# Optimization experiments

Measured on AMD Instinct MI355X. Metric: run time of the kernel, lower is better.

Reference implementation:

```python
import jax, jax.numpy as jnp
import numpy as np
import math

NUM_HEADS = 16
HEAD_DIM = 64
EMBED = 1024
NUM_BUCKETS = 32
MAX_DISTANCE = 128


def _relative_position_bucket(relative_position, num_buckets=NUM_BUCKETS, max_distance=MAX_DISTANCE):
    # bidirectional T5 bucketing
    nb = num_buckets // 2
    relative_buckets = (relative_position > 0).astype(jnp.int32) * nb
    rp = jnp.abs(relative_position)
    max_exact = nb // 2
    is_small = rp < max_exact
    rp_safe = jnp.maximum(rp, 1)  # avoid log(0); masked by is_small anyway
    rp_large = max_exact + (
        jnp.log(rp_safe.astype(jnp.float32) / max_exact)
        / math.log(max_distance / max_exact)
        * (nb - max_exact)
    ).astype(jnp.int32)
    rp_large = jnp.minimum(rp_large, nb - 1)
    return relative_buckets + jnp.where(is_small, rp, rp_large)


def compute_bias(rel_emb, q_len, k_len):
    ctx = jnp.arange(q_len)[:, None]
    mem = jnp.arange(k_len)[None, :]
    buckets = _relative_position_bucket(mem - ctx)  # [q,k]
    values = rel_emb[buckets]                       # [q,k,H]
    return jnp.transpose(values, (2, 0, 1))[None]   # [1,H,q,k]


def setup_inputs() -> dict:
    key = jax.random.key(0)
    ks = jax.random.split(key, 6)
    std = 0.02
    B, S = 2, 2048
    inner = NUM_HEADS * HEAD_DIM
    return {
        "input_ids": jax.random.normal(ks[0], (B, S, EMBED), dtype=jnp.float32),
        "Wq": jax.random.normal(ks[1], (EMBED, inner), dtype=jnp.float32) * std,
        "Wk": jax.random.normal(ks[2], (EMBED, inner), dtype=jnp.float32) * std,
        "Wv": jax.random.normal(ks[3], (EMBED, inner), dtype=jnp.float32) * std,
        "Wo": jax.random.normal(ks[4], (inner, EMBED), dtype=jnp.float32) * std,
        "rel_emb": jax.random.normal(ks[5], (NUM_BUCKETS, NUM_HEADS), dtype=jnp.float32) * std,
    }


def reference(input_ids, Wq, Wk, Wv, Wo, rel_emb):
    B, S, _ = input_ids.shape
    H, D = NUM_HEADS, HEAD_DIM
    q = (input_ids @ Wq).reshape(B, S, H, D).transpose(0, 2, 1, 3)  # [B,H,S,D]
    k = (input_ids @ Wk).reshape(B, S, H, D).transpose(0, 2, 1, 3)
    v = (input_ids @ Wv).reshape(B, S, H, D).transpose(0, 2, 1, 3)
    scores = jnp.einsum("bhqd,bhkd->bhqk", q, k)  # no 1/sqrt(d) scaling (T5 style)
    position_bias = compute_bias(rel_emb, S, S)   # [1,H,S,S]
    scores = scores + position_bias
    attn = jax.nn.softmax(scores, axis=-1)
    out = jnp.einsum("bhqk,bhkd->bhqd", attn, v)
    out = out.transpose(0, 2, 1, 3).reshape(B, S, H * D)
    out = out @ Wo
    return out, position_bias
```

## Files before the change

kernel.cpp:

```cpp
#include <hip/hip_runtime.h>
#include <stdint.h>

#define S_LEN 2048
#define NH 16
#define EMB 1024

typedef __attribute__((ext_vector_type(8))) short bf16x8;
typedef __attribute__((ext_vector_type(4))) float floatx4;
typedef const __attribute__((address_space(1))) unsigned int* gas_u32p;
typedef __attribute__((address_space(3))) unsigned int* las_u32p;

static __device__ __forceinline__ void gld_lds16(const void* g, void* l) {
  __builtin_amdgcn_global_load_lds((gas_u32p)g, (las_u32p)l, 16, 0, 0);
}

static __device__ __forceinline__ unsigned short f2bf(float f) {
  unsigned int u = __float_as_uint(f);
  unsigned int r = (u + 0x7FFFu + ((u >> 16) & 1u)) >> 16;
  return (unsigned short)r;
}

__global__ void cast_x_kernel(const float* __restrict__ x, unsigned short* __restrict__ out, int n4) {
  int i = blockIdx.x * blockDim.x + threadIdx.x;
  if (i >= n4) return;
  float4 v = ((const float4*)x)[i];
  ushort4 o;
  o.x = f2bf(v.x); o.y = f2bf(v.y); o.z = f2bf(v.z); o.w = f2bf(v.w);
  ((ushort4*)out)[i] = o;
}

__global__ void transpose_cast3(const float* __restrict__ W0, const float* __restrict__ W1,
                                const float* __restrict__ W2, unsigned short* __restrict__ out) {
  __shared__ float tile[32][33];
  const float* in = (blockIdx.z == 0) ? W0 : ((blockIdx.z == 1) ? W1 : W2);
  unsigned short* o = out + (size_t)blockIdx.z * 1048576;
  int x = blockIdx.x * 32 + threadIdx.x;
  int y0 = blockIdx.y * 32 + threadIdx.y;
#pragma unroll
  for (int j = 0; j < 4; j++)
    tile[threadIdx.y + 8 * j][threadIdx.x] = in[(y0 + 8 * j) * EMB + x];
  __syncthreads();
  int x2 = blockIdx.y * 32 + threadIdx.x;
  int y2 = blockIdx.x * 32 + threadIdx.y;
#pragma unroll
  for (int j = 0; j < 4; j++)
    o[(y2 + 8 * j) * EMB + x2] = f2bf(tile[threadIdx.x][threadIdx.y + 8 * j]);
}

__global__ void build_lut_kernel(const float* __restrict__ rel_emb, float* __restrict__ lut) {
  int idx = blockIdx.x * blockDim.x + threadIdx.x;
  if (idx >= 4096) return;
  int delta = idx - 2048;
  int bucket = (delta > 0) ? 16 : 0;
  int rp = (delta < 0) ? -delta : delta;
  int bl;
  if (rp < 8) bl = rp;
  else bl = 8 + (rp >= 12) + (rp >= 16) + (rp >= 23) + (rp >= 32) + (rp >= 46) + (rp >= 64) + (rp >= 91);
  bucket += bl;
#pragma unroll
  for (int h = 0; h < NH; h++)
    lut[h * 4096 + idx] = rel_emb[bucket * NH + h];
}

__global__ void bias_out_kernel(const float* __restrict__ lut, float* __restrict__ dst) {
  int i = blockIdx.x * blockDim.x + threadIdx.x;
  int h = i >> 20;
  int rem = i & 1048575;
  int q = rem >> 9;
  int k4 = (rem & 511) << 2;
  const float* lr = lut + h * 4096 + (k4 - q + 2048);
  float4 v = make_float4(__ldg(lr), __ldg(lr + 1), __ldg(lr + 2), __ldg(lr + 3));
  ((float4*)dst)[i] = v;
}

template <int MODE>
__global__ __launch_bounds__(256) void gemm2(const unsigned short* __restrict__ A,
                                             const unsigned short* __restrict__ BT,
                                             unsigned short* __restrict__ oQ,
                                             unsigned short* __restrict__ oK,
                                             unsigned short* __restrict__ oV,
                                             float* __restrict__ oF) {
  __shared__ __align__(16) unsigned short As[128 * 64];
  __shared__ __align__(16) unsigned short Bs[128 * 64];
  const int tid = threadIdx.x;
  const int wave = tid >> 6, lane = tid & 63;
  const int quad = lane >> 4, lm = lane & 15;
  const int wm = wave & 1, wn = wave >> 1;
  const int mBase = blockIdx.y * 128, nBase = blockIdx.x * 128;
  const int gg = (lane & 7) ^ (lane >> 3);
  const int srow = lane >> 3;
  floatx4 acc[4][4];
#pragma unroll
  for (int i = 0; i < 4; i++)
#pragma unroll
    for (int j = 0; j < 4; j++) acc[i][j] = (floatx4){0.f, 0.f, 0.f, 0.f};

  for (int kt = 0; kt < 16; kt++) {
    int k0 = kt * 64;
    __syncthreads();
#pragma unroll
    for (int c = 0; c < 4; c++) {
      int chunk = wave * 4 + c;
      int row = chunk * 8 + srow;
      gld_lds16(&A[(size_t)(mBase + row) * 1024 + k0 + gg * 8], &As[chunk * 512]);
      gld_lds16(&BT[(size_t)(nBase + row) * 1024 + k0 + gg * 8], &Bs[chunk * 512]);
    }
    __syncthreads();
#pragma unroll
    for (int hh = 0; hh < 2; hh++) {
      bf16x8 af[4], bfr[4];
#pragma unroll
      for (int i = 0; i < 4; i++)
        af[i] = *(const bf16x8*)&As[(wm * 64 + i * 16 + lm) * 64 + (((hh << 2) + quad) ^ (lm & 7)) * 8];
#pragma unroll
      for (int j = 0; j < 4; j++)
        bfr[j] = *(const bf16x8*)&Bs[(wn * 64 + j * 16 + lm) * 64 + (((hh << 2) + quad) ^ (lm & 7)) * 8];
#pragma unroll
      for (int i = 0; i < 4; i++)
#pragma unroll
        for (int j = 0; j < 4; j++)
          acc[i][j] = __builtin_amdgcn_mfma_f32_16x16x32_bf16(af[i], bfr[j], acc[i][j], 0, 0, 0);
    }
  }
  const int which = nBase >> 10;
#pragma unroll
  for (int i = 0; i < 4; i++) {
#pragma unroll
    for (int j = 0; j < 4; j++) {
#pragma unroll
      for (int r = 0; r < 4; r++) {
        int row = mBase + wm * 64 + i * 16 + quad * 4 + r;
        int col = nBase + wn * 64 + j * 16 + lm;
        float v = acc[i][j][r];
        if (MODE == 1) {
          oF[(size_t)row * 1024 + col] = v;
        } else {
          int b = row >> 11, s = row & 2047;
          int cw = col & 1023;
          int h = cw >> 6, d = cw & 63;
          if (which == 0)      oQ[(((size_t)(b * NH + h) * S_LEN + s) * 64) + d] = f2bf(v);
          else if (which == 1) oK[(((size_t)(b * NH + h) * S_LEN + s) * 64) + d] = f2bf(v);
          else                 oV[(((size_t)(b * NH + h) * 64 + d) * S_LEN) + s] = f2bf(v);
        }
      }
    }
  }
}

__global__ __launch_bounds__(256) void attn_kernel(const unsigned short* __restrict__ Qb,
                                                   const unsigned short* __restrict__ Kb,
                                                   const unsigned short* __restrict__ Vtb,
                                                   const float* __restrict__ lut,
                                                   unsigned short* __restrict__ Ob) {
  __shared__ __align__(16) unsigned short Kl[64 * 64];
  __shared__ __align__(16) unsigned short Vl[64 * 64];
  __shared__ __align__(16) unsigned short Pl[4 * 16 * 72];
  const int tid = threadIdx.x;
  const int wave = tid >> 6, lane = tid & 63;
  const int quad = lane >> 4, lm = lane & 15;
  const int h = blockIdx.y, b = blockIdx.z;
  const int bh = b * NH + h;
  const int qTile = blockIdx.x * 128;
  const unsigned short* Qp = Qb + (size_t)bh * S_LEN * 64;
  const unsigned short* Kp = Kb + (size_t)bh * S_LEN * 64;
  const unsigned short* Vp = Vtb + (size_t)bh * 64 * S_LEN;
  const float* lrow = lut + h * 4096;
  const float cneg = lrow[0], cpos = lrow[4095];
  const int gg = (lane & 7) ^ (lane >> 3);
  const int srow = lane >> 3;
  const int qw = qTile + wave * 32;

  bf16x8 aq[2][2];
#pragma unroll
  for (int g = 0; g < 2; g++)
#pragma unroll
    for (int hh = 0; hh < 2; hh++)
      aq[g][hh] = *(const bf16x8*)&Qp[(qw + g * 16 + lm) * 64 + hh * 32 + quad * 8];

  floatx4 accO[2][4];
#pragma unroll
  for (int g = 0; g < 2; g++)
#pragma unroll
    for (int d = 0; d < 4; d++) accO[g][d] = (floatx4){0.f, 0.f, 0.f, 0.f};
  float lp[2] = {0.f, 0.f};

  unsigned short* Pw = &Pl[wave * 16 * 72];

  for (int kt = 0; kt < 32; kt++) {
    int kBase = kt * 64;
    __syncthreads();
#pragma unroll
    for (int c = 0; c < 2; c++) {
      int chunk = wave * 2 + c;
      int row = chunk * 8 + srow;
      gld_lds16(&Kp[(size_t)(kBase + row) * 64 + gg * 8], &Kl[chunk * 512]);
      gld_lds16(&Vp[(size_t)row * S_LEN + kBase + gg * 8], &Vl[chunk * 512]);
    }
    __syncthreads();

    bf16x8 kf[4][2], vf[4][2];
#pragma unroll
    for (int nt = 0; nt < 4; nt++)
#pragma unroll
      for (int hh = 0; hh < 2; hh++) {
        int off = (nt * 16 + lm) * 64 + (((hh << 2) + quad) ^ (lm & 7)) * 8;
        kf[nt][hh] = *(const bf16x8*)&Kl[off];
        vf[nt][hh] = *(const bf16x8*)&Vl[off];
      }

    bool farTile = (kBase + 154 <= qTile) || (kBase >= qTile + 218);
    float cfar = (kBase < qTile) ? cneg : cpos;

#pragma unroll
    for (int g = 0; g < 2; g++) {
      int q = qw + g * 16 + lm;
      floatx4 s4[4];
#pragma unroll
      for (int nt = 0; nt < 4; nt++) {
        floatx4 z = (floatx4){0.f, 0.f, 0.f, 0.f};
        z = __builtin_amdgcn_mfma_f32_16x16x32_bf16(kf[nt][0], aq[g][0], z, 0, 0, 0);
        z = __builtin_amdgcn_mfma_f32_16x16x32_bf16(kf[nt][1], aq[g][1], z, 0, 0, 0);
        s4[nt] = z;
      }
      float psum = 0.f;
#pragma unroll
      for (int nt = 0; nt < 4; nt++) {
        union { unsigned short u[4]; uint2 v; } pk;
#pragma unroll
        for (int r = 0; r < 4; r++) {
          float sv;
          if (farTile) sv = s4[nt][r] + cfar;
          else {
            int kcol = kBase + nt * 16 + quad * 4 + r;
            sv = s4[nt][r] + __ldg(&lrow[kcol - q + 2048]);
          }
          float p = __expf(sv);
          psum += p;
          pk.u[r] = f2bf(p);
        }
        *(uint2*)&Pw[lm * 72 + nt * 16 + quad * 4] = pk.v;
      }
      lp[g] += psum;
      bf16x8 pa0 = *(const bf16x8*)&Pw[lm * 72 + quad * 8];
      bf16x8 pa1 = *(const bf16x8*)&Pw[lm * 72 + 32 + quad * 8];
#pragma unroll
      for (int d = 0; d < 4; d++) {
        accO[g][d] = __builtin_amdgcn_mfma_f32_16x16x32_bf16(pa0, vf[d][0], accO[g][d], 0, 0, 0);
        accO[g][d] = __builtin_amdgcn_mfma_f32_16x16x32_bf16(pa1, vf[d][1], accO[g][d], 0, 0, 0);
      }
    }
  }
#pragma unroll
  for (int g = 0; g < 2; g++) {
    lp[g] += __shfl_xor(lp[g], 16, 64);
    lp[g] += __shfl_xor(lp[g], 32, 64);
  }
#pragma unroll
  for (int g = 0; g < 2; g++) {
    float linv[4];
#pragma unroll
    for (int r = 0; r < 4; r++) linv[r] = 1.f / __shfl(lp[g], quad * 4 + r, 64);
#pragma unroll
    for (int d = 0; d < 4; d++)
#pragma unroll
      for (int r = 0; r < 4; r++) {
        int q = qw + g * 16 + quad * 4 + r;
        int col = h * 64 + d * 16 + lm;
        Ob[((size_t)(b * S_LEN + q)) * 1024 + col] = f2bf(accO[g][d][r] * linv[r]);
      }
  }
}

extern "C" void kernel_launch(void* const* d_in, const int* in_sizes, int n_in,
                              void* d_out, int out_size, void* d_ws, size_t ws_size,
                              hipStream_t stream) {
  const float* X   = (const float*)d_in[0];
  const float* Wq  = (const float*)d_in[1];
  const float* Wk  = (const float*)d_in[2];
  const float* Wv  = (const float*)d_in[3];
  const float* Wo  = (const float*)d_in[4];
  const float* rel = (const float*)d_in[5];
  float* out = (float*)d_out;
  float* bias_out = out + 4194304;

  char* ws = (char*)d_ws;
  unsigned short* Xb    = (unsigned short*)(ws);
  unsigned short* WqkvT = (unsigned short*)(ws + (size_t)(8u  << 20));
  unsigned short* WoT   = (unsigned short*)(ws + (size_t)(14u << 20));
  unsigned short* Qb    = (unsigned short*)(ws + (size_t)(16u << 20));
  unsigned short* Kb    = (unsigned short*)(ws + (size_t)(24u << 20));
  unsigned short* Vtb   = (unsigned short*)(ws + (size_t)(32u << 20));
  unsigned short* Ob    = (unsigned short*)(ws + (size_t)(40u << 20));
  float* lut            = (float*)(ws + (size_t)(48u << 20));

  cast_x_kernel<<<4096, 256, 0, stream>>>(X, Xb, 1048576);
  dim3 tb(32, 8);
  transpose_cast3<<<dim3(32, 32, 3), tb, 0, stream>>>(Wq, Wk, Wv, WqkvT);
  transpose_cast3<<<dim3(32, 32, 1), tb, 0, stream>>>(Wo, Wo, Wo, WoT);
  build_lut_kernel<<<16, 256, 0, stream>>>(rel, lut);
  bias_out_kernel<<<65536, 256, 0, stream>>>(lut, bias_out);

  gemm2<0><<<dim3(24, 32), 256, 0, stream>>>(Xb, WqkvT, Qb, Kb, Vtb, nullptr);
  attn_kernel<<<dim3(16, 16, 2), 256, 0, stream>>>(Qb, Kb, Vtb, lut, Ob);
  gemm2<1><<<dim3(8, 32), 256, 0, stream>>>(Ob, WoT, nullptr, nullptr, nullptr, out);
}
```

Measured before the change: 478.9 us.

## Fuse bias output into attention, split QKV GEMM, remap attention grid

Removes the standalone position-bias kernel. The batch-0 attention blocks now write the bias tile for each key block with nontemporal stores, using a constant fill for far tiles. The QKV GEMM is split into a Q/K kernel and a separate V kernel whose MFMA operands are swapped so the transposed V store is coalesced along s. Attention blocks are remapped to a 1D grid that interleaves batch and head, the P scratch pitch changes from 72 to 68, and a cheaper round-half-up bf16 conversion is used for P and O. Risks include extra store traffic inside attention for batch-0 blocks, load imbalance between the two batches, and slightly different rounding.

```diff
diff --git a/kernel.cpp b/kernel.cpp
--- a/kernel.cpp
+++ b/kernel.cpp
@@ -18,6 +18,9 @@
   unsigned int u = __float_as_uint(f);
   unsigned int r = (u + 0x7FFFu + ((u >> 16) & 1u)) >> 16;
   return (unsigned short)r;
+}
+static __device__ __forceinline__ unsigned short f2bf_fast(float f) {
+  return (unsigned short)((__float_as_uint(f) + 0x8000u) >> 16);
 }
 
 __global__ void cast_x_kernel(const float* __restrict__ x, unsigned short* __restrict__ out, int n4) {
@@ -62,24 +65,10 @@
     lut[h * 4096 + idx] = rel_emb[bucket * NH + h];
 }
 
-__global__ void bias_out_kernel(const float* __restrict__ lut, float* __restrict__ dst) {
-  int i = blockIdx.x * blockDim.x + threadIdx.x;
-  int h = i >> 20;
-  int rem = i & 1048575;
-  int q = rem >> 9;
-  int k4 = (rem & 511) << 2;
-  const float* lr = lut + h * 4096 + (k4 - q + 2048);
-  float4 v = make_float4(__ldg(lr), __ldg(lr + 1), __ldg(lr + 2), __ldg(lr + 3));
-  ((float4*)dst)[i] = v;
-}
-
-template <int MODE>
-__global__ __launch_bounds__(256) void gemm2(const unsigned short* __restrict__ A,
-                                             const unsigned short* __restrict__ BT,
-                                             unsigned short* __restrict__ oQ,
-                                             unsigned short* __restrict__ oK,
-                                             unsigned short* __restrict__ oV,
-                                             float* __restrict__ oF) {
+__global__ __launch_bounds__(256) void gemm_qk(const unsigned short* __restrict__ A,
+                                               const unsigned short* __restrict__ BT,
+                                               unsigned short* __restrict__ oQ,
+                                               unsigned short* __restrict__ oK) {
   __shared__ __align__(16) unsigned short As[128 * 64];
   __shared__ __align__(16) unsigned short Bs[128 * 64];
   const int tid = threadIdx.x;
@@ -124,43 +113,154 @@
   }
   const int which = nBase >> 10;
 #pragma unroll
-  for (int i = 0; i < 4; i++) {
-#pragma unroll
-    for (int j = 0; j < 4; j++) {
+  for (int i = 0; i < 4; i++)
+#pragma unroll
+    for (int j = 0; j < 4; j++)
 #pragma unroll
       for (int r = 0; r < 4; r++) {
         int row = mBase + wm * 64 + i * 16 + quad * 4 + r;
         int col = nBase + wn * 64 + j * 16 + lm;
-        float v = acc[i][j][r];
-        if (MODE == 1) {
-          oF[(size_t)row * 1024 + col] = v;
-        } else {
-          int b = row >> 11, s = row & 2047;
-          int cw = col & 1023;
-          int h = cw >> 6, d = cw & 63;
-          if (which == 0)      oQ[(((size_t)(b * NH + h) * S_LEN + s) * 64) + d] = f2bf(v);
-          else if (which == 1) oK[(((size_t)(b * NH + h) * S_LEN + s) * 64) + d] = f2bf(v);
-          else                 oV[(((size_t)(b * NH + h) * 64 + d) * S_LEN) + s] = f2bf(v);
-        }
-      }
-    }
-  }
+        int b = row >> 11, s = row & 2047;
+        int cw = col & 1023;
+        int h = cw >> 6, d = cw & 63;
+        unsigned short v = f2bf(acc[i][j][r]);
+        if (which == 0) oQ[(((size_t)(b * NH + h) * S_LEN + s) * 64) + d] = v;
+        else            oK[(((size_t)(b * NH + h) * S_LEN + s) * 64) + d] = v;
+      }
+}
+
+__global__ __launch_bounds__(256) void gemm_v(const unsigned short* __restrict__ A,
+                                              const unsigned short* __restrict__ BT,
+                                              unsigned short* __restrict__ oV) {
+  __shared__ __align__(16) unsigned short As[128 * 64];
+  __shared__ __align__(16) unsigned short Bs[128 * 64];
+  const int tid = threadIdx.x;
+  const int wave = tid >> 6, lane = tid & 63;
+  const int quad = lane >> 4, lm = lane & 15;
+  const int wm = wave & 1, wn = wave >> 1;
+  const int mBase = blockIdx.y * 128, nBase = blockIdx.x * 128;
+  const int gg = (lane & 7) ^ (lane >> 3);
+  const int srow = lane >> 3;
+  floatx4 acc[4][4];
+#pragma unroll
+  for (int i = 0; i < 4; i++)
+#pragma unroll
+    for (int j = 0; j < 4; j++) acc[i][j] = (floatx4){0.f, 0.f, 0.f, 0.f};
+
+  for (int kt = 0; kt < 16; kt++) {
+    int k0 = kt * 64;
+    __syncthreads();
+#pragma unroll
+    for (int c = 0; c < 4; c++) {
+      int chunk = wave * 4 + c;
+      int row = chunk * 8 + srow;
+      gld_lds16(&A[(size_t)(mBase + row) * 1024 + k0 + gg * 8], &As[chunk * 512]);
+      gld_lds16(&BT[(size_t)(nBase + row) * 1024 + k0 + gg * 8], &Bs[chunk * 512]);
+    }
+    __syncthreads();
+#pragma unroll
+    for (int hh = 0; hh < 2; hh++) {
+      bf16x8 af[4], bfr[4];
+#pragma unroll
+      for (int i = 0; i < 4; i++)
+        af[i] = *(const bf16x8*)&As[(wm * 64 + i * 16 + lm) * 64 + (((hh << 2) + quad) ^ (lm & 7)) * 8];
+#pragma unroll
+      for (int j = 0; j < 4; j++)
+        bfr[j] = *(const bf16x8*)&Bs[(wn * 64 + j * 16 + lm) * 64 + (((hh << 2) + quad) ^ (lm & 7)) * 8];
+#pragma unroll
+      for (int i = 0; i < 4; i++)
+#pragma unroll
+        for (int j = 0; j < 4; j++)
+          acc[i][j] = __builtin_amdgcn_mfma_f32_16x16x32_bf16(bfr[j], af[i], acc[i][j], 0, 0, 0);
+    }
+  }
+#pragma unroll
+  for (int i = 0; i < 4; i++)
+#pragma unroll
+    for (int j = 0; j < 4; j++)
+#pragma unroll
+      for (int r = 0; r < 4; r++) {
+        int n = nBase + wn * 64 + j * 16 + quad * 4 + r;
+        int m = mBase + wm * 64 + i * 16 + lm;
+        int h = n >> 6, d = n & 63;
+        int b = m >> 11, s = m & 2047;
+        oV[(((size_t)(b * NH + h) * 64 + d) * S_LEN) + s] = f2bf(acc[i][j][r]);
+      }
+}
+
+__global__ __launch_bounds__(256) void gemm_out(const unsigned short* __restrict__ A,
+                                                const unsigned short* __restrict__ BT,
+                                                float* __restrict__ oF) {
+  __shared__ __align__(16) unsigned short As[128 * 64];
+  __shared__ __align__(16) unsigned short Bs[128 * 64];
+  const int tid = threadIdx.x;
+  const int wave = tid >> 6, lane = tid & 63;
+  const int quad = lane >> 4, lm = lane & 15;
+  const int wm = wave & 1, wn = wave >> 1;
+  const int mBase = blockIdx.y * 128, nBase = blockIdx.x * 128;
+  const int gg = (lane & 7) ^ (lane >> 3);
+  const int srow = lane >> 3;
+  floatx4 acc[4][4];
+#pragma unroll
+  for (int i = 0; i < 4; i++)
+#pragma unroll
+    for (int j = 0; j < 4; j++) acc[i][j] = (floatx4){0.f, 0.f, 0.f, 0.f};
+
+  for (int kt = 0; kt < 16; kt++) {
+    int k0 = kt * 64;
+    __syncthreads();
+#pragma unroll
+    for (int c = 0; c < 4; c++) {
+      int chunk = wave * 4 + c;
+      int row = chunk * 8 + srow;
+      gld_lds16(&A[(size_t)(mBase + row) * 1024 + k0 + gg * 8], &As[chunk * 512]);
+      gld_lds16(&BT[(size_t)(nBase + row) * 1024 + k0 + gg * 8], &Bs[chunk * 512]);
+    }
+    __syncthreads();
+#pragma unroll
+    for (int hh = 0; hh < 2; hh++) {
+      bf16x8 af[4], bfr[4];
+#pragma unroll
+      for (int i = 0; i < 4; i++)
+        af[i] = *(const bf16x8*)&As[(wm * 64 + i * 16 + lm) * 64 + (((hh << 2) + quad) ^ (lm & 7)) * 8];
+#pragma unroll
+      for (int j = 0; j < 4; j++)
+        bfr[j] = *(const bf16x8*)&Bs[(wn * 64 + j * 16 + lm) * 64 + (((hh << 2) + quad) ^ (lm & 7)) * 8];
+#pragma unroll
+      for (int i = 0; i < 4; i++)
+#pragma unroll
+        for (int j = 0; j < 4; j++)
+          acc[i][j] = __builtin_amdgcn_mfma_f32_16x16x32_bf16(af[i], bfr[j], acc[i][j], 0, 0, 0);
+    }
+  }
+#pragma unroll
+  for (int i = 0; i < 4; i++)
+#pragma unroll
+    for (int j = 0; j < 4; j++)
+#pragma unroll
+      for (int r = 0; r < 4; r++) {
+        int row = mBase + wm * 64 + i * 16 + quad * 4 + r;
+        int col = nBase + wn * 64 + j * 16 + lm;
+        oF[(size_t)row * 1024 + col] = acc[i][j][r];
+      }
 }
 
 __global__ __launch_bounds__(256) void attn_kernel(const unsigned short* __restrict__ Qb,
                                                    const unsigned short* __restrict__ Kb,
                                                    const unsigned short* __restrict__ Vtb,
                                                    const float* __restrict__ lut,
-                                                   unsigned short* __restrict__ Ob) {
+                                                   unsigned short* __restrict__ Ob,
+                                                   float* __restrict__ bias_out) {
   __shared__ __align__(16) unsigned short Kl[64 * 64];
   __shared__ __align__(16) unsigned short Vl[64 * 64];
-  __shared__ __align__(16) unsigned short Pl[4 * 16 * 72];
+  __shared__ __align__(16) unsigned short Pl[4 * 16 * 68];
   const int tid = threadIdx.x;
   const int wave = tid >> 6, lane = tid & 63;
   const int quad = lane >> 4, lm = lane & 15;
-  const int h = blockIdx.y, b = blockIdx.z;
-  const int bh = b * NH + h;
-  const int qTile = blockIdx.x * 128;
+  const int ii = blockIdx.x;
+  const int bh = (ii & 7) * 4 + ((ii >> 3) & 3);
+  const int qTile = (ii >> 5) * 128;
+  const int b = bh >> 4, h = bh & 15;
   const unsigned short* Qp = Qb + (size_t)bh * S_LEN * 64;
   const unsigned short* Kp = Kb + (size_t)bh * S_LEN * 64;
   const unsigned short* Vp = Vtb + (size_t)bh * 64 * S_LEN;
@@ -169,6 +269,8 @@
   const int gg = (lane & 7) ^ (lane >> 3);
   const int srow = lane >> 3;
   const int qw = qTile + wave * 32;
+  const bool writeBias = (b == 0);
+  float* bdst = bias_out + ((size_t)(h * S_LEN + qTile)) * S_LEN;
 
   bf16x8 aq[2][2];
 #pragma unroll
@@ -184,7 +286,7 @@
     for (int d = 0; d < 4; d++) accO[g][d] = (floatx4){0.f, 0.f, 0.f, 0.f};
   float lp[2] = {0.f, 0.f};
 
-  unsigned short* Pw = &Pl[wave * 16 * 72];
+  unsigned short* Pw = &Pl[wave * 16 * 68];
 
   for (int kt = 0; kt < 32; kt++) {
     int kBase = kt * 64;
@@ -198,6 +300,31 @@
     }
     __syncthreads();
 
+    bool farTile = (kBase + 154 <= qTile) || (kBase >= qTile + 218);
+    float cfar = (kBase < qTile) ? cneg : cpos;
+
+    if (writeBias) {
+      float* bt = bdst + kBase;
+      if (farTile) {
+        floatx4 cf4 = (floatx4){cfar, cfar, cfar, cfar};
+#pragma unroll
+        for (int e = 0; e < 8; e++) {
+          int f = tid + e * 256;
+          int qlo = f >> 4, kk = (f & 15) << 2;
+          __builtin_nontemporal_store(cf4, (floatx4*)&bt[(size_t)qlo * S_LEN + kk]);
+        }
+      } else {
+#pragma unroll
+        for (int e = 0; e < 8; e++) {
+          int f = tid + e * 256;
+          int qlo = f >> 4, kk = (f & 15) << 2;
+          const float* lr = lrow + (kBase + kk) - (qTile + qlo) + 2048;
+          floatx4 v = (floatx4){lr[0], lr[1], lr[2], lr[3]};
+          __builtin_nontemporal_store(v, (floatx4*)&bt[(size_t)qlo * S_LEN + kk]);
+        }
+      }
+    }
+
     bf16x8 kf[4][2], vf[4][2];
 #pragma unroll
     for (int nt = 0; nt < 4; nt++)
@@ -207,9 +334,6 @@
         kf[nt][hh] = *(const bf16x8*)&Kl[off];
         vf[nt][hh] = *(const bf16x8*)&Vl[off];
       }
-
-    bool farTile = (kBase + 154 <= qTile) || (kBase >= qTile + 218);
-    float cfar = (kBase < qTile) ? cneg : cpos;
 
 #pragma unroll
     for (int g = 0; g < 2; g++) {
@@ -236,13 +360,13 @@
           }
           float p = __expf(sv);
           psum += p;
-          pk.u[r] = f2bf(p);
+          pk.u[r] = f2bf_fast(p);
         }
-        *(uint2*)&Pw[lm * 72 + nt * 16 + quad * 4] = pk.v;
+        *(uint2*)&Pw[lm * 68 + nt * 16 + quad * 4] = pk.v;
       }
       lp[g] += psum;
-      bf16x8 pa0 = *(const bf16x8*)&Pw[lm * 72 + quad * 8];
-      bf16x8 pa1 = *(const bf16x8*)&Pw[lm * 72 + 32 + quad * 8];
+      bf16x8 pa0 = *(const bf16x8*)&Pw[lm * 68 + quad * 8];
+      bf16x8 pa1 = *(const bf16x8*)&Pw[lm * 68 + 32 + quad * 8];
 #pragma unroll
       for (int d = 0; d < 4; d++) {
         accO[g][d] = __builtin_amdgcn_mfma_f32_16x16x32_bf16(pa0, vf[d][0], accO[g][d], 0, 0, 0);
@@ -264,9 +388,9 @@
     for (int d = 0; d < 4; d++)
 #pragma unroll
       for (int r = 0; r < 4; r++) {
-        int q = qw + g * 16 + quad * 4 + r;
+        int q = qTile + wave * 32 + g * 16 + quad * 4 + r;
         int col = h * 64 + d * 16 + lm;
-        Ob[((size_t)(b * S_LEN + q)) * 1024 + col] = f2bf(accO[g][d][r] * linv[r]);
+        Ob[((size_t)(b * S_LEN + q)) * 1024 + col] = f2bf_fast(accO[g][d][r] * linv[r]);
       }
   }
 }
@@ -298,9 +422,9 @@
   transpose_cast3<<<dim3(32, 32, 3), tb, 0, stream>>>(Wq, Wk, Wv, WqkvT);
   transpose_cast3<<<dim3(32, 32, 1), tb, 0, stream>>>(Wo, Wo, Wo, WoT);
   build_lut_kernel<<<16, 256, 0, stream>>>(rel, lut);
-  bias_out_kernel<<<65536, 256, 0, stream>>>(lut, bias_out);
-
-  gemm2<0><<<dim3(24, 32), 256, 0, stream>>>(Xb, WqkvT, Qb, Kb, Vtb, nullptr);
-  attn_kernel<<<dim3(16, 16, 2), 256, 0, stream>>>(Qb, Kb, Vtb, lut, Ob);
-  gemm2<1><<<dim3(8, 32), 256, 0, stream>>>(Ob, WoT, nullptr, nullptr, nullptr, out);
-}
+
+  gemm_qk<<<dim3(16, 32), 256, 0, stream>>>(Xb, WqkvT, Qb, Kb);
+  gemm_v<<<dim3(8, 32), 256, 0, stream>>>(Xb, WqkvT + 2 * 1048576, Vtb);
+  attn_kernel<<<512, 256, 0, stream>>>(Qb, Kb, Vtb, lut, Ob, bias_out);
+  gemm_out<<<dim3(8, 32), 256, 0, stream>>>(Ob, WoT, out);
+}
```

Result: slower. 515.7 us (+7.7%).
